# Performance work log

Hardware: AMD Instinct MI355X
Metric: run time of the kernel (lower is better)

The kernel has to match this reference:

```python
import jax, jax.numpy as jnp
import numpy as np

C = 1024
H = 16
D = C // H  # head_dim = 64
FF = 4 * C


def setup_inputs() -> dict:
    key = jax.random.key(0)
    ks = jax.random.split(key, 10)
    s = lambda fan_in: 1.0 / np.sqrt(fan_in)
    return {
        "x": jax.random.normal(ks[0], (2, 2048, C), dtype=jnp.float32),
        "ln1_g": jnp.ones((C,), jnp.float32),
        "ln1_b": jnp.zeros((C,), jnp.float32),
        "w_qkv": jax.random.normal(ks[1], (C, 3 * C), jnp.float32) * s(C),
        "w_proj": jax.random.normal(ks[2], (C, C), jnp.float32) * s(C),
        "b_proj": jnp.zeros((C,), jnp.float32),
        "ln2_g": jnp.ones((C,), jnp.float32),
        "ln2_b": jnp.zeros((C,), jnp.float32),
        "w_fc1": jax.random.normal(ks[3], (C, FF), jnp.float32) * s(C),
        "b_fc1": jnp.zeros((FF,), jnp.float32),
        "w_fc2": jax.random.normal(ks[4], (FF, C), jnp.float32) * s(FF),
        "b_fc2": jnp.zeros((C,), jnp.float32),
    }


def _layernorm(x, g, b, eps=1e-5):
    mu = jnp.mean(x, axis=-1, keepdims=True)
    var = jnp.var(x, axis=-1, keepdims=True)
    return (x - mu) * jax.lax.rsqrt(var + eps) * g + b


def reference(x, ln1_g, ln1_b, w_qkv, w_proj, b_proj, ln2_g, ln2_b, w_fc1, b_fc1, w_fc2, b_fc2):
    B, N, _ = x.shape
    scale = D ** -0.5
    # --- attention sub-block (pre-LN) ---
    h = _layernorm(x, ln1_g, ln1_b)
    qkv = (h @ w_qkv).reshape(B, N, 3, H, D)
    q, k, v = jnp.moveaxis(qkv, 2, 0)          # each [B, N, H, D]
    attn = jnp.einsum("bnhd,bmhd->bhnm", q, k) * scale  # [B,H,N,N]
    attn = jax.nn.softmax(attn, axis=-1)
    o = jnp.einsum("bhnm,bmhd->bnhd", attn, v).reshape(B, N, C)
    x = x + o @ w_proj + b_proj
    # --- MLP sub-block (pre-LN) ---
    h = _layernorm(x, ln2_g, ln2_b)
    h = jax.nn.gelu(h @ w_fc1 + b_fc1, approximate=False)
    x = x + h @ w_fc2 + b_fc2
    return x
```

## Files before the change

kernel.cpp:

```cpp
#include <hip/hip_runtime.h>
#include <hip/hip_bf16.h>

typedef unsigned short u16;
typedef unsigned int u32;
typedef __attribute__((ext_vector_type(8))) short bf16x8;
typedef __attribute__((ext_vector_type(4))) float f32x4;
typedef __attribute__((ext_vector_type(4))) int   i32x4;
typedef __attribute__((ext_vector_type(4))) float fvec4;

__device__ inline u16 f2bf(float f) {
    union { float f; unsigned u; } v; v.f = f;
    unsigned r = v.u + 0x7fffu + ((v.u >> 16) & 1u);
    return (u16)(r >> 16);
}

__device__ inline f32x4 mfma16(bf16x8 a, bf16x8 b, f32x4 c) {
    return __builtin_amdgcn_mfma_f32_16x16x32_bf16(a, b, c, 0, 0, 0);
}

__device__ inline void gload16(const void* g, void* l) {
    __builtin_amdgcn_global_load_lds(
        (const __attribute__((address_space(1))) unsigned int*)g,
        (__attribute__((address_space(3))) unsigned int*)l, 16, 0, 0);
}

__global__ __launch_bounds__(256)
void transpose_all(const float* __restrict__ w0, u16* __restrict__ o0,
                   const float* __restrict__ w1, u16* __restrict__ o1,
                   const float* __restrict__ w2, u16* __restrict__ o2,
                   const float* __restrict__ w3, u16* __restrict__ o3) {
    __shared__ float tile[32][33];
    int b = blockIdx.x;
    const float* in; u16* out; int K, N, local;
    if (b < 3072)      { in = w0; out = o0; K = 1024; N = 3072; local = b; }
    else if (b < 4096) { in = w1; out = o1; K = 1024; N = 1024; local = b - 3072; }
    else if (b < 8192) { in = w2; out = o2; K = 1024; N = 4096; local = b - 4096; }
    else               { in = w3; out = o3; K = 4096; N = 1024; local = b - 8192; }
    const int nx = N >> 5;
    const int n0 = (local % nx) * 32, k0 = (local / nx) * 32;
    const int x = threadIdx.x & 31, y = threadIdx.x >> 5;
    for (int i = 0; i < 4; ++i)
        tile[y + i * 8][x] = in[(size_t)(k0 + y + i * 8) * N + n0 + x];
    __syncthreads();
    for (int i = 0; i < 4; ++i) {
        int r = y + i * 8;
        out[(size_t)(n0 + r) * K + k0 + x] = f2bf(tile[x][r]);
    }
}

__global__ __launch_bounds__(256)
void vtrans(const u16* __restrict__ qkv, u16* __restrict__ vT) {
    __shared__ u32 tl[64][33];
    const int t0 = blockIdx.x * 64, f0 = blockIdx.y * 64;
    const int a = threadIdx.x & 31, yy = threadIdx.x >> 5;
    for (int i = 0; i < 8; ++i) {
        int t = yy + i * 8;
        tl[t][a] = *(const u32*)(qkv + (size_t)(t0 + t) * 3072 + 2048 + f0 + a * 2);
    }
    __syncthreads();
    for (int i = 0; i < 8; ++i) {
        int f = yy + i * 8;
        u32 lo = tl[2 * a][f >> 1], hi = tl[2 * a + 1][f >> 1];
        u32 r = (f & 1) ? ((lo >> 16) | (hi & 0xffff0000u))
                        : ((lo & 0xffffu) | (hi << 16));
        *(u32*)(vT + (size_t)(f0 + f) * 4096 + t0 + 2 * a) = r;
    }
}

__global__ __launch_bounds__(256)
void ln_kernel(const float* __restrict__ x, const float* __restrict__ g,
               const float* __restrict__ bvec, u16* __restrict__ out) {
    __shared__ float red[2][4];
    const int row = blockIdx.x, tid = threadIdx.x;
    const float* xr = x + (size_t)row * 1024;
    fvec4 v = *(const fvec4*)(xr + tid * 4);
    float s  = v[0] + v[1] + v[2] + v[3];
    float s2 = v[0]*v[0] + v[1]*v[1] + v[2]*v[2] + v[3]*v[3];
    for (int off = 1; off < 64; off <<= 1) {
        s  += __shfl_xor(s,  off);
        s2 += __shfl_xor(s2, off);
    }
    const int w = tid >> 6;
    if ((tid & 63) == 0) { red[0][w] = s; red[1][w] = s2; }
    __syncthreads();
    s  = red[0][0] + red[0][1] + red[0][2] + red[0][3];
    s2 = red[1][0] + red[1][1] + red[1][2] + red[1][3];
    const float mu  = s * (1.0f / 1024.0f);
    const float var = s2 * (1.0f / 1024.0f) - mu * mu;
    const float rstd = rsqrtf(var + 1e-5f);
    fvec4 gv = *(const fvec4*)(g + tid * 4);
    fvec4 bv = *(const fvec4*)(bvec + tid * 4);
    u16 o4[4];
    for (int i = 0; i < 4; ++i)
        o4[i] = f2bf((v[i] - mu) * rstd * gv[i] + bv[i]);
    u32 lo = (u32)o4[0] | ((u32)o4[1] << 16);
    u32 hi = (u32)o4[2] | ((u32)o4[3] << 16);
    u32* dst = (u32*)(out + (size_t)row * 1024 + tid * 4);
    dst[0] = lo; dst[1] = hi;
}

template <int MODE, int WM, int WN, int MT, int NT, int NYP>
__global__ __launch_bounds__(256)
void gemm64(const u16* __restrict__ A, const u16* __restrict__ Bt,
            const float* __restrict__ bias, const float* __restrict__ res,
            void* __restrict__ out, int M, int N, int K) {
    constexpr int TM = WM * MT * 16;
    constexpr int TN = WN * NT * 16;
    constexpr int AJ = TM / 64;
    constexpr int BJ = TN / 64;
    static_assert(TM == 128, "swizzle assumes 32 M-tiles");
    __shared__ __attribute__((aligned(16))) u16 sA[2 * TM * 32];
    __shared__ __attribute__((aligned(16))) u16 sB[2 * TN * 32];
    const int id = blockIdx.x;
    const int j  = id >> 3;
    const int by = (id & 7) * NYP + (j >> 5);
    const int bx = j & 31;
    const int tid = threadIdx.x;
    const int lane = tid & 63, w = tid >> 6;
    const int wm = w / WN, wn = w % WN;
    const int q = lane >> 4, l16 = lane & 15;

    f32x4 acc[MT][NT];
#pragma unroll
    for (int i = 0; i < MT; ++i)
#pragma unroll
        for (int jj = 0; jj < NT; ++jj) acc[i][jj] = (f32x4)0.0f;

    const int sr = lane >> 2;
    const int kc = (lane & 3) * 8;
    const u16* gA[AJ];
    const u16* gB[BJ];
#pragma unroll
    for (int jj = 0; jj < AJ; ++jj)
        gA[jj] = A + (size_t)(bx * TM + (jj * 4 + w) * 16 + sr) * K + kc;
#pragma unroll
    for (int jj = 0; jj < BJ; ++jj)
        gB[jj] = Bt + (size_t)(by * TN + (jj * 4 + w) * 16 + sr) * K + kc;

    for (int k0 = 0; k0 < K; k0 += 64) {
#pragma unroll
        for (int kt = 0; kt < 2; ++kt) {
#pragma unroll
            for (int jj = 0; jj < AJ; ++jj)
                gload16(gA[jj] + k0 + kt * 32, &sA[kt * TM * 32 + (jj * 4 + w) * 512]);
#pragma unroll
            for (int jj = 0; jj < BJ; ++jj)
                gload16(gB[jj] + k0 + kt * 32, &sB[kt * TN * 32 + (jj * 4 + w) * 512]);
        }
        __syncthreads();
#pragma unroll
        for (int kt = 0; kt < 2; ++kt) {
            bf16x8 af[MT], bf[NT];
#pragma unroll
            for (int mt = 0; mt < MT; ++mt)
                af[mt] = *(const bf16x8*)&sA[kt * TM * 32 +
                         (wm * MT * 16 + mt * 16 + l16) * 32 + q * 8];
#pragma unroll
            for (int nt = 0; nt < NT; ++nt)
                bf[nt] = *(const bf16x8*)&sB[kt * TN * 32 +
                         (wn * NT * 16 + nt * 16 + l16) * 32 + q * 8];
#pragma unroll
            for (int mt = 0; mt < MT; ++mt)
#pragma unroll
                for (int nt = 0; nt < NT; ++nt)
                    acc[mt][nt] = mfma16(af[mt], bf[nt], acc[mt][nt]);
        }
        __syncthreads();
    }

#pragma unroll
    for (int mt = 0; mt < MT; ++mt)
#pragma unroll
        for (int nt = 0; nt < NT; ++nt)
#pragma unroll
            for (int r = 0; r < 4; ++r) {
                const int row = bx * TM + wm * MT * 16 + mt * 16 + q * 4 + r;
                const int col = by * TN + wn * NT * 16 + nt * 16 + l16;
                const size_t idx = (size_t)row * N + col;
                float v = acc[mt][nt][r];
                if (MODE == 0) {
                    ((u16*)out)[idx] = f2bf(v);
                } else if (MODE == 1) {
                    ((float*)out)[idx] = v + bias[col] + res[idx];
                } else {
                    float t = v + bias[col];
                    ((u16*)out)[idx] = f2bf(t * 0.5f * (1.0f + erff(t * 0.70710678118f)));
                }
            }
}

template <int MODE>
__global__ __launch_bounds__(512)
void gemm256(const u16* __restrict__ A, const u16* __restrict__ Bt,
             const float* __restrict__ bias, const float* __restrict__ res,
             void* __restrict__ out, int M, int N, int K) {
    __shared__ __attribute__((aligned(16))) u16 sA[2][16384];
    __shared__ __attribute__((aligned(16))) u16 sB[2][16384];
    const int tid  = threadIdx.x;
    const int w    = tid >> 6, lane = tid & 63;
    const int wm   = w >> 2,  wn   = w & 3;
    const int q    = lane >> 4, l16 = lane & 15;
    const int w8   = w << 3,  l8   = lane >> 3;
    const int kch  = (lane & 7) ^ l8;

    const int nwg  = gridDim.x;
    const int id   = blockIdx.x;
    const int wgid = (id & 7) * (nwg >> 3) + (id >> 3);
    const int bx   = wgid & 15, by = wgid >> 4;

    const u16* pAs = A  + (size_t)(bx * 256 + w8 + l8) * K + kch * 8;
    const u16* pBs = Bt + (size_t)(by * 256 + w8 + l8) * K + kch * 8;

    const int cs0  = ((q ^ (l16 & 7)) << 4);
    const int cs1  = cs0 ^ 64;
    const int aoff = (wm * 128 + l16) * 128;
    const int boff = (wn * 64  + l16) * 128;

    f32x4 acc[8][4];
#pragma unroll
    for (int m = 0; m < 8; ++m)
#pragma unroll
        for (int n = 0; n < 4; ++n) acc[m][n] = (f32x4)0.0f;

#define GISS(P, r0, k0, SH, b_) \
    gload16((P) + (size_t)((r0) * K + (k0)), &SH[b_][((r0) + w8) * 64])

    GISS(pBs, 0, 0, sB, 0);  GISS(pBs, 64, 0, sB, 0);
    GISS(pBs, 128, 0, sB, 0); GISS(pBs, 192, 0, sB, 0);
    GISS(pAs, 0, 0, sA, 0);  GISS(pAs, 64, 0, sA, 0);
    GISS(pAs, 128, 0, sA, 0); GISS(pAs, 192, 0, sA, 0);
    GISS(pBs, 0, 64, sB, 1); GISS(pBs, 64, 64, sB, 1);
    GISS(pBs, 128, 64, sB, 1); GISS(pBs, 192, 64, sB, 1);
    asm volatile("s_waitcnt vmcnt(4)" ::: "memory");
    __builtin_amdgcn_s_barrier();

    bf16x8 bfr[4][2];

#define PHASE(mq_, cb_, SP, SH, sb_, sr0, sk0) do {                          \
    const char* bA_ = (const char*)&sA[cb_][0] + aoff;                       \
    const char* bB_ = (const char*)&sB[cb_][0] + boff;                       \
    if ((mq_) == 0) {                                                        \
        _Pragma("unroll") for (int n = 0; n < 4; ++n) {                      \
            bfr[n][0] = *(const bf16x8*)(bB_ + n * 2048 + cs0);              \
            bfr[n][1] = *(const bf16x8*)(bB_ + n * 2048 + cs1);              \
        }                                                                    \
    }                                                                        \
    bf16x8 af_[2][2];                                                        \
    _Pragma("unroll") for (int mi = 0; mi < 2; ++mi) {                       \
        af_[mi][0] = *(const bf16x8*)(bA_ + (2 * (mq_) + mi) * 2048 + cs0);  \
        af_[mi][1] = *(const bf16x8*)(bA_ + (2 * (mq_) + mi) * 2048 + cs1);  \
    }                                                                        \
    GISS(SP, (sr0), (sk0), SH, sb_);                                         \
    GISS(SP, (sr0) + 64, (sk0), SH, sb_);                                    \
    __builtin_amdgcn_s_barrier();                                            \
    __builtin_amdgcn_s_setprio(1);                                           \
    _Pragma("unroll") for (int kt = 0; kt < 2; ++kt)                         \
        _Pragma("unroll") for (int mi = 0; mi < 2; ++mi)                     \
            _Pragma("unroll") for (int n = 0; n < 4; ++n)                    \
                acc[2 * (mq_) + mi][n] =                                     \
                    mfma16(af_[mi][kt], bfr[n][kt], acc[2 * (mq_) + mi][n]); \
    __builtin_amdgcn_s_setprio(0);                                           \
    if ((mq_) == 3) asm volatile("s_waitcnt vmcnt(4)" ::: "memory");         \
    __builtin_amdgcn_s_barrier();                                            \
} while (0)

    const int NI = K >> 7;
    for (int i = 0; i < NI; ++i) {
        const int kb  = i << 7;
        const int kA1 = kb + 64;
        const int kN  = (kb + 128 < K) ? kb + 128 : K - 64;
        const int kB1 = (kb + 192 < K) ? kb + 192 : K - 64;
        PHASE(0, 0, pAs, sA, 1, 0,   kA1);
        PHASE(1, 0, pAs, sA, 1, 128, kA1);
        PHASE(2, 0, pBs, sB, 0, 0,   kN);
        PHASE(3, 0, pBs, sB, 0, 128, kN);
        PHASE(0, 1, pAs, sA, 0, 0,   kN);
        PHASE(1, 1, pAs, sA, 0, 128, kN);
        PHASE(2, 1, pBs, sB, 1, 0,   kB1);
        PHASE(3, 1, pBs, sB, 1, 128, kB1);
    }
#undef PHASE
#undef GISS

#pragma unroll
    for (int m = 0; m < 8; ++m)
#pragma unroll
        for (int n = 0; n < 4; ++n)
#pragma unroll
            for (int r = 0; r < 4; ++r) {
                const int row = bx * 256 + wm * 128 + m * 16 + q * 4 + r;
                const int col = by * 256 + wn * 64 + n * 16 + l16;
                const size_t idx = (size_t)row * N + col;
                float v = acc[m][n][r];
                if (MODE == 0) {
                    ((u16*)out)[idx] = f2bf(v);
                } else if (MODE == 1) {
                    ((float*)out)[idx] = v + bias[col] + res[idx];
                } else {
                    float t = v + bias[col];
                    ((u16*)out)[idx] = f2bf(t * 0.5f * (1.0f + erff(t * 0.70710678118f)));
                }
            }
}

__global__ __launch_bounds__(256)
void attention3(const u16* __restrict__ qkv, const u16* __restrict__ vT,
                u16* __restrict__ o) {
    __shared__ __attribute__((aligned(16))) u16 sK[64][72];
    __shared__ __attribute__((aligned(16))) u16 sV[64][72];

    const int tid = threadIdx.x;
    const int lane = tid & 63, w = tid >> 6;
    const int qc = lane >> 4, l16 = lane & 15;
    const int bx = blockIdx.x;
    const int qt = bx & 15, h = (bx >> 4) & 15, b = bx >> 8;
    const int rowbase = qt * 128 + w * 32;

    bf16x8 aQ[2][2];
#pragma unroll
    for (int mtq = 0; mtq < 2; ++mtq)
#pragma unroll
        for (int kd = 0; kd < 2; ++kd)
            aQ[mtq][kd] = *(const bf16x8*)(qkv +
                (size_t)(b * 2048 + rowbase + mtq * 16 + l16) * 3072 +
                h * 64 + kd * 32 + qc * 8);

    f32x4 accO[2][4];
#pragma unroll
    for (int mtq = 0; mtq < 2; ++mtq)
#pragma unroll
        for (int dt = 0; dt < 4; ++dt) accO[mtq][dt] = (f32x4)0.0f;
    float lsum[2] = {0.0f, 0.0f};

    const int srr = tid >> 3;
    const int sc8 = (tid & 7) * 8;
    const u16* gK = qkv + (size_t)(b * 2048 + srr) * 3072 + 1024 + h * 64 + sc8;
    const u16* gV = vT + (size_t)(h * 64 + srr) * 4096 + b * 2048 + sc8;

    i32x4 cK[2], cV[2];
    cK[0] = *(const i32x4*)gK;
    cK[1] = *(const i32x4*)(gK + (size_t)32 * 3072);
    cV[0] = *(const i32x4*)gV;
    cV[1] = *(const i32x4*)(gV + (size_t)32 * 4096);

    const int sig_base = ((l16 >> 2) << 3) + (l16 & 3);

    for (int kc = 0; kc < 32; ++kc) {
        __syncthreads();
        *(i32x4*)&sK[srr][sc8]      = cK[0];
        *(i32x4*)&sK[srr + 32][sc8] = cK[1];
        *(i32x4*)&sV[srr][sc8]      = cV[0];
        *(i32x4*)&sV[srr + 32][sc8] = cV[1];
        const int kn = (kc + 1 < 32) ? kc + 1 : 31;
        i32x4 nK[2], nV[2];
        nK[0] = *(const i32x4*)(gK + (size_t)kn * 64 * 3072);
        nK[1] = *(const i32x4*)(gK + ((size_t)kn * 64 + 32) * 3072);
        nV[0] = *(const i32x4*)(gV + kn * 64);
        nV[1] = *(const i32x4*)(gV + (size_t)32 * 4096 + kn * 64);
        __syncthreads();

        bf16x8 kf[4][2];
#pragma unroll
        for (int mk = 0; mk < 4; ++mk) {
            const int krow = ((mk & 1) << 5) + ((mk >> 1) << 2) + sig_base;
            kf[mk][0] = *(const bf16x8*)&sK[krow][qc * 8];
            kf[mk][1] = *(const bf16x8*)&sK[krow][32 + qc * 8];
        }

        f32x4 s[2][4];
#pragma unroll
        for (int mtq = 0; mtq < 2; ++mtq)
#pragma unroll
            for (int mk = 0; mk < 4; ++mk) {
                f32x4 z = (f32x4)0.0f;
                z = mfma16(kf[mk][0], aQ[mtq][0], z);
                z = mfma16(kf[mk][1], aQ[mtq][1], z);
                s[mtq][mk] = z;
            }

        bf16x8 pf[2][2];
#pragma unroll
        for (int mtq = 0; mtq < 2; ++mtq) {
            float ls = 0.0f;
#pragma unroll
            for (int mk = 0; mk < 4; ++mk)
#pragma unroll
                for (int r = 0; r < 4; ++r) {
                    float p = __expf(s[mtq][mk][r] * 0.125f);
                    s[mtq][mk][r] = p;
                    ls += p;
                }
            lsum[mtq] += ls;
#pragma unroll
            for (int kt = 0; kt < 2; ++kt)
#pragma unroll
                for (int jj = 0; jj < 4; ++jj) {
                    pf[mtq][kt][jj]     = (short)f2bf(s[mtq][kt][jj]);
                    pf[mtq][kt][4 + jj] = (short)f2bf(s[mtq][2 + kt][jj]);
                }
        }

#pragma unroll
        for (int kt = 0; kt < 2; ++kt)
#pragma unroll
            for (int dt = 0; dt < 4; ++dt) {
                bf16x8 vf = *(const bf16x8*)&sV[dt * 16 + l16][kt * 32 + qc * 8];
#pragma unroll
                for (int mtq = 0; mtq < 2; ++mtq)
                    accO[mtq][dt] = mfma16(pf[mtq][kt], vf, accO[mtq][dt]);
            }

        cK[0] = nK[0]; cK[1] = nK[1];
        cV[0] = nV[0]; cV[1] = nV[1];
    }

#pragma unroll
    for (int mtq = 0; mtq < 2; ++mtq) {
        lsum[mtq] += __shfl_xor(lsum[mtq], 16);
        lsum[mtq] += __shfl_xor(lsum[mtq], 32);
    }

#pragma unroll
    for (int mtq = 0; mtq < 2; ++mtq)
#pragma unroll
        for (int r = 0; r < 4; ++r) {
            const float lr = __shfl(lsum[mtq], qc * 4 + r, 16);
            const float inv = 1.0f / lr;
            const size_t tok = (size_t)b * 2048 + rowbase + mtq * 16 + qc * 4 + r;
#pragma unroll
            for (int dt = 0; dt < 4; ++dt)
                o[tok * 1024 + h * 64 + dt * 16 + l16] = f2bf(accO[mtq][dt][r] * inv);
        }
}

extern "C" void kernel_launch(void* const* d_in, const int* in_sizes, int n_in,
                              void* d_out, int out_size, void* d_ws, size_t ws_size,
                              hipStream_t stream) {
    const float* x      = (const float*)d_in[0];
    const float* ln1_g  = (const float*)d_in[1];
    const float* ln1_b  = (const float*)d_in[2];
    const float* w_qkv  = (const float*)d_in[3];
    const float* w_proj = (const float*)d_in[4];
    const float* b_proj = (const float*)d_in[5];
    const float* ln2_g  = (const float*)d_in[6];
    const float* ln2_b  = (const float*)d_in[7];
    const float* w_fc1  = (const float*)d_in[8];
    const float* b_fc1  = (const float*)d_in[9];
    const float* w_fc2  = (const float*)d_in[10];
    const float* b_fc2  = (const float*)d_in[11];
    float* out = (float*)d_out;

    char* ws = (char*)d_ws;
    u16*   wqkvT  = (u16*)(ws + 0);
    u16*   wprojT = (u16*)(ws + 6291456);
    u16*   wfc1T  = (u16*)(ws + 8388608);
    u16*   wfc2T  = (u16*)(ws + 16777216);
    u16*   hA     = (u16*)(ws + 25165824);
    u16*   qkv    = (u16*)(ws + 33554432);
    float* x1     = (float*)(ws + 58720256);
    u16*   gbuf   = (u16*)(ws + 75497472);
    u16*   vT     = (u16*)(ws + 75497472);

    dim3 blk(256);
    transpose_all<<<12288, blk, 0, stream>>>(w_qkv, wqkvT, w_proj, wprojT,
                                             w_fc1, wfc1T, w_fc2, wfc2T);

    ln_kernel<<<4096, blk, 0, stream>>>(x, ln1_g, ln1_b, hA);
    gemm256<0><<<192, dim3(512), 0, stream>>>(hA, wqkvT, nullptr, nullptr, qkv, 4096, 3072, 1024);
    vtrans<<<dim3(64, 16), blk, 0, stream>>>(qkv, vT);
    attention3<<<512, blk, 0, stream>>>(qkv, vT, hA);
    gemm64<1, 4, 1, 2, 4, 2><<<512, blk, 0, stream>>>(hA, wprojT, b_proj, x, x1, 4096, 1024, 1024);

    u16* h2 = qkv;
    ln_kernel<<<4096, blk, 0, stream>>>(x1, ln2_g, ln2_b, h2);
    gemm256<2><<<256, dim3(512), 0, stream>>>(h2, wfc1T, b_fc1, nullptr, gbuf, 4096, 4096, 1024);
    gemm64<1, 4, 1, 2, 4, 2><<<512, blk, 0, stream>>>(gbuf, wfc2T, b_fc2, x1, out, 4096, 1024, 4096);
}
```

Baseline: 361.5 us.

## Split-K the FC2 GEMM onto 256-tile kernel with separate reduction pass

Result: no change. 355.8 us (-1.6%).

```diff
diff --git a/kernel.cpp b/kernel.cpp
--- a/kernel.cpp
+++ b/kernel.cpp
@@ -99,6 +99,23 @@
     dst[0] = lo; dst[1] = hi;
 }
 
+__global__ __launch_bounds__(256)
+void reduce4(const float* __restrict__ p1, const float* __restrict__ p2,
+             const float* __restrict__ p3, const float* __restrict__ bias,
+             const float* __restrict__ res, float* __restrict__ out) {
+    const size_t base = (size_t)blockIdx.x * 1024 + threadIdx.x * 4;
+    fvec4 a = *(const fvec4*)(out + base);
+    fvec4 b = *(const fvec4*)(p1 + base);
+    fvec4 c = *(const fvec4*)(p2 + base);
+    fvec4 d = *(const fvec4*)(p3 + base);
+    fvec4 r = *(const fvec4*)(res + base);
+    fvec4 bi = *(const fvec4*)(bias + threadIdx.x * 4);
+    fvec4 o;
+#pragma unroll
+    for (int i = 0; i < 4; ++i) o[i] = ((a[i] + b[i]) + (c[i] + d[i])) + bi[i] + r[i];
+    *(fvec4*)(out + base) = o;
+}
+
 template <int MODE, int WM, int WN, int MT, int NT, int NYP>
 __global__ __launch_bounds__(256)
 void gemm64(const u16* __restrict__ A, const u16* __restrict__ Bt,
@@ -189,11 +206,13 @@
             }
 }
 
-template <int MODE>
+template <int MODE, int SPLIT>
 __global__ __launch_bounds__(512)
 void gemm256(const u16* __restrict__ A, const u16* __restrict__ Bt,
              const float* __restrict__ bias, const float* __restrict__ res,
-             void* __restrict__ out, int M, int N, int K) {
+             void* __restrict__ out,
+             float* __restrict__ q1, float* __restrict__ q2, float* __restrict__ q3,
+             int M, int N, int K, int Kc) {
     __shared__ __attribute__((aligned(16))) u16 sA[2][16384];
     __shared__ __attribute__((aligned(16))) u16 sB[2][16384];
     const int tid  = threadIdx.x;
@@ -206,10 +225,12 @@
     const int nwg  = gridDim.x;
     const int id   = blockIdx.x;
     const int wgid = (id & 7) * (nwg >> 3) + (id >> 3);
-    const int bx   = wgid & 15, by = wgid >> 4;
-
-    const u16* pAs = A  + (size_t)(bx * 256 + w8 + l8) * K + kch * 8;
-    const u16* pBs = Bt + (size_t)(by * 256 + w8 + l8) * K + kch * 8;
+    int bx, by, sp;
+    if (SPLIT == 1) { bx = wgid & 15; by = wgid >> 4; sp = 0; }
+    else            { bx = wgid & 15; by = (wgid >> 4) & 3; sp = wgid >> 6; }
+
+    const u16* pAs = A  + (size_t)(bx * 256 + w8 + l8) * K + kch * 8 + (size_t)sp * Kc;
+    const u16* pBs = Bt + (size_t)(by * 256 + w8 + l8) * K + kch * 8 + (size_t)sp * Kc;
 
     const int cs0  = ((q ^ (l16 & 7)) << 4);
     const int cs1  = cs0 ^ 64;
@@ -252,7 +273,10 @@
     }                                                                        \
     GISS(SP, (sr0), (sk0), SH, sb_);                                         \
     GISS(SP, (sr0) + 64, (sk0), SH, sb_);                                    \
+    __builtin_amdgcn_sched_barrier(0);   \
     __builtin_amdgcn_s_barrier();                                            \
+    asm volatile("s_waitcnt lgkmcnt(0)" ::: "memory");                       \
+    __builtin_amdgcn_sched_barrier(0);          \
     __builtin_amdgcn_s_setprio(1);                                           \
     _Pragma("unroll") for (int kt = 0; kt < 2; ++kt)                         \
         _Pragma("unroll") for (int mi = 0; mi < 2; ++mi)                     \
@@ -264,12 +288,12 @@
     __builtin_amdgcn_s_barrier();                                            \
 } while (0)
 
-    const int NI = K >> 7;
+    const int NI = Kc >> 7;
     for (int i = 0; i < NI; ++i) {
         const int kb  = i << 7;
         const int kA1 = kb + 64;
-        const int kN  = (kb + 128 < K) ? kb + 128 : K - 64;
-        const int kB1 = (kb + 192 < K) ? kb + 192 : K - 64;
+        const int kN  = (kb + 128 < Kc) ? kb + 128 : Kc - 64;
+        const int kB1 = (kb + 192 < Kc) ? kb + 192 : Kc - 64;
         PHASE(0, 0, pAs, sA, 1, 0,   kA1);
         PHASE(1, 0, pAs, sA, 1, 128, kA1);
         PHASE(2, 0, pBs, sB, 0, 0,   kN);
@@ -281,6 +305,10 @@
     }
 #undef PHASE
 #undef GISS
+
+    float* po = nullptr;
+    if (MODE == 3)
+        po = sp == 0 ? (float*)out : sp == 1 ? q1 : sp == 2 ? q2 : q3;
 
 #pragma unroll
     for (int m = 0; m < 8; ++m)
@@ -296,9 +324,11 @@
                     ((u16*)out)[idx] = f2bf(v);
                 } else if (MODE == 1) {
                     ((float*)out)[idx] = v + bias[col] + res[idx];
-                } else {
+                } else if (MODE == 2) {
                     float t = v + bias[col];
                     ((u16*)out)[idx] = f2bf(t * 0.5f * (1.0f + erff(t * 0.70710678118f)));
+                } else {
+                    po[idx] = v;
                 }
             }
 }
@@ -460,19 +490,26 @@
     float* x1     = (float*)(ws + 58720256);
     u16*   gbuf   = (u16*)(ws + 75497472);
     u16*   vT     = (u16*)(ws + 75497472);
+    float* p1     = (float*)(ws + 0);
+    float* p2     = (float*)(ws + 25165824);
+    float* p3     = (float*)(ws + 41943040);
 
     dim3 blk(256);
     transpose_all<<<12288, blk, 0, stream>>>(w_qkv, wqkvT, w_proj, wprojT,
                                              w_fc1, wfc1T, w_fc2, wfc2T);
 
     ln_kernel<<<4096, blk, 0, stream>>>(x, ln1_g, ln1_b, hA);
-    gemm256<0><<<192, dim3(512), 0, stream>>>(hA, wqkvT, nullptr, nullptr, qkv, 4096, 3072, 1024);
+    gemm256<0, 1><<<192, dim3(512), 0, stream>>>(hA, wqkvT, nullptr, nullptr, qkv,
+                                                 nullptr, nullptr, nullptr, 4096, 3072, 1024, 1024);
     vtrans<<<dim3(64, 16), blk, 0, stream>>>(qkv, vT);
     attention3<<<512, blk, 0, stream>>>(qkv, vT, hA);
     gemm64<1, 4, 1, 2, 4, 2><<<512, blk, 0, stream>>>(hA, wprojT, b_proj, x, x1, 4096, 1024, 1024);
 
     u16* h2 = qkv;
     ln_kernel<<<4096, blk, 0, stream>>>(x1, ln2_g, ln2_b, h2);
-    gemm256<2><<<256, dim3(512), 0, stream>>>(h2, wfc1T, b_fc1, nullptr, gbuf, 4096, 4096, 1024);
-    gemm64<1, 4, 1, 2, 4, 2><<<512, blk, 0, stream>>>(gbuf, wfc2T, b_fc2, x1, out, 4096, 1024, 4096);
-}
+    gemm256<2, 1><<<256, dim3(512), 0, stream>>>(h2, wfc1T, b_fc1, nullptr, gbuf,
+                                                 nullptr, nullptr, nullptr, 4096, 4096, 1024, 1024);
+    gemm256<3, 4><<<256, dim3(512), 0, stream>>>(gbuf, wfc2T, nullptr, nullptr, out,
+                                                 p1, p2, p3, 4096, 1024, 4096, 1024);
+    reduce4<<<4096, blk, 0, stream>>>(p1, p2, p3, b_fc2, x1, out);
+}
```
